# Optimization experiments

Hardware: AMD Instinct MI355X
Metric: run time of the kernel (lower is better)

## Reference

```python
import jax, jax.numpy as jnp
import numpy as np

D = 768       # model dim
H = 12        # num heads
DH = 64       # hidden_dim per head (D == H*DH)
DT = 32       # time_dim
KTEMP = 1.0   # k_temperature
LN_EPS = 1e-5


def setup_inputs() -> dict:
    key = jax.random.key(0)
    ks = jax.random.split(key, 10)
    B, T = 2, 2048
    states = jax.random.normal(ks[0], (B, T, D), jnp.float32)
    attention_mask = jnp.ones((B, T), jnp.int32)
    s = 0.02
    Wq = jax.random.normal(ks[1], (H * DH, D), jnp.float32) * s
    Wk = jax.random.normal(ks[2], (H * DH, D), jnp.float32) * s
    bk = jax.random.normal(ks[3], (H * DH,), jnp.float32) * s
    Wv = jax.random.normal(ks[4], (H * DH, D), jnp.float32) * s
    bv = jnp.zeros((H * DH,), jnp.float32)           # V.bias zeroed in __init__
    Wo = jax.random.normal(ks[5], (D, H * DH), jnp.float32) * s
    bo = jnp.zeros((D,), jnp.float32)                # O.bias zeroed in __init__
    q_bias = jnp.zeros((H * DH,), jnp.float32)
    time_angle = jax.random.uniform(ks[6], (H, DT), jnp.float32) ** 10 + 1e-8
    head_time_delta = jax.random.uniform(ks[7], (H,), jnp.float32)
    ln_gamma = jnp.ones((D,), jnp.float32)
    ln_beta = jnp.zeros((D,), jnp.float32)
    return {"states": states, "attention_mask": attention_mask,
            "Wq": Wq, "Wk": Wk, "bk": bk, "Wv": Wv, "bv": bv,
            "Wo": Wo, "bo": bo, "q_bias": q_bias,
            "time_angle": time_angle, "head_time_delta": head_time_delta,
            "ln_gamma": ln_gamma, "ln_beta": ln_beta}


def reference(states, attention_mask, Wq, Wk, bk, Wv, bv, Wo, bo, q_bias,
              time_angle, head_time_delta, ln_gamma, ln_beta):
    B, T, _ = states.shape
    dtype = states.dtype
    mask = attention_mask.astype(dtype)[..., None, None]  # B T 1 1

    inv_sqrt_dh = 1.0 / np.sqrt(DH).astype(np.float32)

    def get_time(delta):
        # delta: [1,H,1] or scalar 0.0
        pos = jnp.arange(T, dtype=dtype)[:, None, None]     # T 1 1
        ang = (pos + delta) * time_angle[None]              # T H Dt
        c, s = jnp.cos(ang), jnp.sin(ang)
        return jnp.concatenate([c + s, c - s], axis=-1) * inv_sqrt_dh  # T H 2Dt

    # --- q path ---
    q = states @ Wq.T - jnp.exp(q_bias)                     # B T (H*Dh), Q has no bias
    q = jax.nn.sigmoid(q.reshape(B, T, H, DH)) / DH * mask  # B T H Dh
    time_q = get_time(head_time_delta[None, :, None])       # T H 2Dt (with delta)
    time_k = get_time(0.0)                                  # T H 2Dt
    q_timed = q.sum(-1, keepdims=True) * time_q             # B T H 2Dt
    # scores: B T(query) L(key) H -- the large materialized tensor
    scores = jnp.einsum('bthd,lhd->btlh', q_timed, time_k)

    # --- kv path ---
    k = (states @ Wk.T + bk).reshape(B, T, H, DH) / KTEMP * mask
    v = (states @ Wv.T + bv).reshape(B, T, H, DH)
    kv = jax.nn.softmax(k, axis=-1) * v                     # B T H Dh

    # --- aggregate ---
    loading = jnp.einsum('btlh,blhd->bthd', scores, kv).reshape(B, T, D)
    attn_out = loading @ Wo.T + bo

    # residual + layernorm (dropout is identity in eval)
    x = states + attn_out
    mu = x.mean(-1, keepdims=True)
    var = x.var(-1, keepdims=True)
    return (x - mu) * jax.lax.rsqrt(var + LN_EPS) * ln_gamma + ln_beta
```

## Files before the change

kernel.cpp:

```cpp
#include <hip/hip_runtime.h>
#include <math.h>
#include <stdint.h>

#define TT 2048
#define BB 2
#define DD 768
#define HH 12
#define DHH 64
#define DTT 32
#define NROW 4096

typedef float v4 __attribute__((ext_vector_type(4)));
typedef __attribute__((ext_vector_type(8))) short s8v;
typedef __attribute__((ext_vector_type(4))) float f4v;
typedef unsigned short u16;
typedef __attribute__((ext_vector_type(4))) unsigned short us4;

__device__ __forceinline__ float wave_sum(float v) {
#pragma unroll
  for (int m = 32; m > 0; m >>= 1) v += __shfl_xor(v, m, 64);
  return v;
}
__device__ __forceinline__ float wave_max(float v) {
#pragma unroll
  for (int m = 32; m > 0; m >>= 1) v = fmaxf(v, __shfl_xor(v, m, 64));
  return v;
}
__device__ __forceinline__ u16 f2bf(float x) {
  unsigned u = __builtin_bit_cast(unsigned, x);
  u += 0x7fffu + ((u >> 16) & 1u);
  return (u16)(u >> 16);
}
__device__ __forceinline__ float bf2f(u16 b) {
  return __builtin_bit_cast(float, (unsigned)b << 16);
}
__device__ __forceinline__ void gload16(const void* g, void* l) {
  __builtin_amdgcn_global_load_lds(
      (const __attribute__((address_space(1))) unsigned int*)g,
      (__attribute__((address_space(3))) unsigned int*)l, 16, 0, 0);
}

__global__ __launch_bounds__(256) void time_tables(
    const float* __restrict__ tang, const float* __restrict__ hdelta,
    u16* __restrict__ timeqb, float* __restrict__ timek) {
  int idx = blockIdx.x * 256 + threadIdx.x;
  if (idx >= TT * HH * DTT) return;
  int d = idx % DTT;
  int h = (idx / DTT) % HH;
  int t = idx / (DTT * HH);
  float ang = tang[h * DTT + d];
  float sk, ck, sq, cq;
  sincosf((float)t * ang, &sk, &ck);
  sincosf(((float)t + hdelta[h]) * ang, &sq, &cq);
  timek[t * DD + h * DHH + d]       = (ck + sk) * 0.125f;
  timek[t * DD + h * DHH + d + DTT] = (ck - sk) * 0.125f;
  timeqb[t * DD + h * DHH + d]       = f2bf((cq + sq) * 0.125f);
  timeqb[t * DD + h * DHH + d + DTT] = f2bf((cq - sq) * 0.125f);
}

__global__ __launch_bounds__(256) void convert_bf16(
    const float* __restrict__ s, const float* __restrict__ wq,
    const float* __restrict__ wk, const float* __restrict__ wv,
    const float* __restrict__ wo, u16* __restrict__ sb,
    u16* __restrict__ wqkvb, u16* __restrict__ wob) {
  int idx = (blockIdx.x * 256 + threadIdx.x) * 4;
  const float* src;
  u16* dst;
  int off;
  if (idx < 3145728) { src = s; dst = sb; off = idx; }
  else if (idx < 3735552) { src = wq; dst = wqkvb; off = idx - 3145728; }
  else if (idx < 4325376) { src = wk; dst = wqkvb + 589824; off = idx - 3735552; }
  else if (idx < 4915200) { src = wv; dst = wqkvb + 1179648; off = idx - 4325376; }
  else { src = wo; dst = wob; off = idx - 4915200; }
  v4 f = *(const v4*)&src[off];
  us4 o;
#pragma unroll
  for (int j = 0; j < 4; ++j) o[j] = f2bf(f[j]);
  *(us4*)&dst[off] = o;
}

template <int EPI, int OBF>
__global__ __launch_bounds__(256) void gemm_bt(
    const u16* __restrict__ A, const u16* __restrict__ B, void* __restrict__ Cv,
    const float* __restrict__ bias, const float* __restrict__ res,
    int M, int N, int K) {
  __shared__ __align__(16) u16 As[2][4096];
  __shared__ __align__(16) u16 Bs[2][4096];
  const int tid = threadIdx.x;
  const int l = tid & 63;
  const int w = tid >> 6;
  const int wr = w >> 1, wc = w & 1;
  const int i0 = blockIdx.y * 128, j0 = blockIdx.x * 128;
  const int srow = tid >> 2, scol = (tid & 3) * 8;
  const u16* gA0 = A + (size_t)(i0 + srow) * K + scol;
  const u16* gA1 = gA0 + (size_t)64 * K;
  const u16* gB0 = B + (size_t)(j0 + srow) * K + scol;
  const u16* gB1 = gB0 + (size_t)64 * K;
  const int lo = tid * 8;

  f4v acc[4][4];
#pragma unroll
  for (int m = 0; m < 4; ++m)
#pragma unroll
    for (int n = 0; n < 4; ++n) acc[m][n] = (f4v){0.f, 0.f, 0.f, 0.f};

  gload16(gA0, &As[0][lo]);
  gload16(gA1, &As[0][2048 + lo]);
  gload16(gB0, &Bs[0][lo]);
  gload16(gB1, &Bs[0][2048 + lo]);

  const int KT = K >> 5;
  const int ar = wr * 64 + (l & 15);
  const int br = wc * 64 + (l & 15);
  const int kx = (l >> 4) * 8;
  int cur = 0;
  for (int kt = 0; kt < KT; ++kt) {
    __syncthreads();
    if (kt + 1 < KT) {
      int kb = (kt + 1) << 5;
      int nb = cur ^ 1;
      gload16(gA0 + kb, &As[nb][lo]);
      gload16(gA1 + kb, &As[nb][2048 + lo]);
      gload16(gB0 + kb, &Bs[nb][lo]);
      gload16(gB1 + kb, &Bs[nb][2048 + lo]);
    }
    s8v af[4], bf[4];
#pragma unroll
    for (int m = 0; m < 4; ++m)
      af[m] = *(const s8v*)&As[cur][(ar + m * 16) * 32 + kx];
#pragma unroll
    for (int n = 0; n < 4; ++n)
      bf[n] = *(const s8v*)&Bs[cur][(br + n * 16) * 32 + kx];
#pragma unroll
    for (int m = 0; m < 4; ++m)
#pragma unroll
      for (int n = 0; n < 4; ++n)
        acc[m][n] =
            __builtin_amdgcn_mfma_f32_16x16x32_bf16(af[m], bf[n], acc[m][n], 0, 0, 0);
    __syncthreads();
    cur ^= 1;
  }

  const int crow = i0 + wr * 64 + (l >> 4) * 4;
  const int ccol = j0 + wc * 64 + (l & 15);
#pragma unroll
  for (int m = 0; m < 4; ++m)
#pragma unroll
    for (int n = 0; n < 4; ++n) {
      int col = ccol + n * 16;
      size_t base = (size_t)(crow + m * 16) * N + col;
#pragma unroll
      for (int r = 0; r < 4; ++r) {
        float vv = acc[m][n][r];
        if (EPI) vv += bias[col] + res[base + (size_t)r * N];
        if (OBF)
          ((u16*)Cv)[base + (size_t)r * N] = f2bf(vv);
        else
          ((float*)Cv)[base + (size_t)r * N] = vv;
      }
    }
}

__global__ __launch_bounds__(256) void fuse_qkv(
    const u16* __restrict__ qkvb, const float* __restrict__ bk,
    const float* __restrict__ bv, const float* __restrict__ qb,
    const int* __restrict__ amask, float* __restrict__ kvout,
    float* __restrict__ qsum) {
  int w = (blockIdx.x << 2) + (threadIdx.x >> 6);
  int lane = threadIdx.x & 63;
  if (w >= NROW * HH) return;
  int h = w % HH;
  int i = w / HH;
  float mk = (float)amask[i];
  const u16* row = qkvb + (size_t)i * 2304;
  int col = h * DHH + lane;
  float qraw = bf2f(row[col]) - expf(qb[col]);
  float q = (1.f / (1.f + expf(-qraw))) * (1.0f / 64.0f) * mk;
  float qs = wave_sum(q);
  if (lane == 0) qsum[i * HH + h] = qs;
  float kval = (bf2f(row[768 + col]) + bk[col]) * mk;
  float kmax = wave_max(kval);
  float e = expf(kval - kmax);
  float es = wave_sum(e);
  float p = e / es;
  float vval = bf2f(row[1536 + col]) + bv[col];
  kvout[((size_t)i * HH + h) * DHH + lane] = p * vval;
}

__global__ __launch_bounds__(256) void calc_M(
    const float* __restrict__ timek, const float* __restrict__ kv,
    float* __restrict__ Mpart) {
  int blk = blockIdx.x;
  int split = blk & 15;
  int bh = blk >> 4;
  int b = bh / HH, h = bh % HH;
  __shared__ float Tk[64][68];
  __shared__ float Kv[64][68];
  int tid = threadIdx.x;
  int tx = tid & 15, ty = tid >> 4;
  float acc[4][4] = {};
  int t0 = split * 128;
  for (int tt = 0; tt < 128; tt += 64) {
#pragma unroll
    for (int p = 0; p < 4; ++p) {
      int f = tid + 256 * p;
      int r = f >> 4, c4 = (f & 15) << 2;
      int t = t0 + tt + r;
      *(v4*)&Tk[r][c4] = *(const v4*)&timek[(size_t)t * DD + h * DHH + c4];
      *(v4*)&Kv[r][c4] =
          *(const v4*)&kv[((size_t)(b * TT + t) * HH + h) * DHH + c4];
    }
    __syncthreads();
#pragma unroll
    for (int kk = 0; kk < 64; ++kk) {
      v4 a = *(const v4*)&Tk[kk][ty * 4];
      v4 bv4 = *(const v4*)&Kv[kk][tx * 4];
#pragma unroll
      for (int r = 0; r < 4; ++r)
#pragma unroll
        for (int c = 0; c < 4; ++c) acc[r][c] += a[r] * bv4[c];
    }
    __syncthreads();
  }
#pragma unroll
  for (int r = 0; r < 4; ++r)
#pragma unroll
    for (int c = 0; c < 4; ++c)
      Mpart[(size_t)blk * 4096 + (tx * 4 + c) * 64 + (ty * 4 + r)] = acc[r][c];
}

__global__ __launch_bounds__(256) void reduce_M(
    const float* __restrict__ Mpart, float* __restrict__ Mt) {
  int idx = blockIdx.x * 256 + threadIdx.x;
  int bh = idx >> 12;
  int p = idx & 4095;
  float s = 0.f;
#pragma unroll
  for (int sp = 0; sp < 16; ++sp)
    s += Mpart[(size_t)((bh << 4) + sp) * 4096 + p];
  Mt[(size_t)bh * 4096 + p] = s;
}

__global__ __launch_bounds__(256) void calc_loading_mfma(
    const u16* __restrict__ timeqb, const float* __restrict__ Mt,
    const float* __restrict__ qsum, u16* __restrict__ loading) {
  const int bh = blockIdx.y;
  const int b = bh / HH, h = bh % HH;
  const int t0 = blockIdx.x * 128;
  __shared__ __align__(16) u16 Ms[64 * 72];
  for (int p = threadIdx.x; p < 4096; p += 256)
    Ms[(p >> 6) * 72 + (p & 63)] = f2bf(Mt[(size_t)bh * 4096 + p]);
  __syncthreads();
  const int l = threadIdx.x & 63, w = threadIdx.x >> 6;
  f4v acc[2][4];
#pragma unroll
  for (int m = 0; m < 2; ++m)
#pragma unroll
    for (int n = 0; n < 4; ++n) acc[m][n] = (f4v){0.f, 0.f, 0.f, 0.f};
  const int arow = t0 + w * 32 + (l & 15);
  const int dcol = l & 15;
#pragma unroll
  for (int ks = 0; ks < 2; ++ks) {
    const int k0 = ks * 32 + (l >> 4) * 8;
    s8v af[2], bf[4];
#pragma unroll
    for (int m = 0; m < 2; ++m)
      af[m] = *(const s8v*)&timeqb[(size_t)(arow + m * 16) * DD + h * DHH + k0];
#pragma unroll
    for (int n = 0; n < 4; ++n)
      bf[n] = *(const s8v*)&Ms[(dcol + n * 16) * 72 + k0];
#pragma unroll
    for (int m = 0; m < 2; ++m)
#pragma unroll
      for (int n = 0; n < 4; ++n)
        acc[m][n] =
            __builtin_amdgcn_mfma_f32_16x16x32_bf16(af[m], bf[n], acc[m][n], 0, 0, 0);
  }
  const int trow = t0 + w * 32 + (l >> 4) * 4;
  float qs[2][4];
#pragma unroll
  for (int m = 0; m < 2; ++m)
#pragma unroll
    for (int r = 0; r < 4; ++r)
      qs[m][r] = qsum[(b * TT + trow + m * 16 + r) * HH + h];
#pragma unroll
  for (int m = 0; m < 2; ++m)
#pragma unroll
    for (int n = 0; n < 4; ++n)
#pragma unroll
      for (int r = 0; r < 4; ++r) {
        int i = b * TT + trow + m * 16 + r;
        loading[(size_t)i * DD + h * DHH + n * 16 + (l & 15)] =
            f2bf(qs[m][r] * acc[m][n][r]);
      }
}

__global__ __launch_bounds__(256) void layernorm(
    const float* __restrict__ X, const float* __restrict__ gamma,
    const float* __restrict__ beta, float* __restrict__ out) {
  int i = blockIdx.x;
  const float* x = X + (size_t)i * 768;
  float vals[3];
  float s = 0.f, s2 = 0.f;
#pragma unroll
  for (int p = 0; p < 3; ++p) {
    float v = x[threadIdx.x + 256 * p];
    vals[p] = v;
    s += v;
    s2 += v * v;
  }
  s = wave_sum(s);
  s2 = wave_sum(s2);
  __shared__ float red[8];
  int w = threadIdx.x >> 6;
  if ((threadIdx.x & 63) == 0) {
    red[w] = s;
    red[4 + w] = s2;
  }
  __syncthreads();
  float stot = red[0] + red[1] + red[2] + red[3];
  float s2tot = red[4] + red[5] + red[6] + red[7];
  float mu = stot * (1.f / 768.f);
  float var = s2tot * (1.f / 768.f) - mu * mu;
  float rs = rsqrtf(var + 1e-5f);
#pragma unroll
  for (int p = 0; p < 3; ++p) {
    int j = threadIdx.x + 256 * p;
    out[(size_t)i * 768 + j] = (vals[p] - mu) * rs * gamma[j] + beta[j];
  }
}

extern "C" void kernel_launch(void* const* d_in, const int* in_sizes, int n_in,
                              void* d_out, int out_size, void* d_ws,
                              size_t ws_size, hipStream_t stream) {
  const float* states = (const float*)d_in[0];
  const int* amask    = (const int*)d_in[1];
  const float* Wq     = (const float*)d_in[2];
  const float* Wk     = (const float*)d_in[3];
  const float* bk     = (const float*)d_in[4];
  const float* Wv     = (const float*)d_in[5];
  const float* bv     = (const float*)d_in[6];
  const float* Wo     = (const float*)d_in[7];
  const float* bo     = (const float*)d_in[8];
  const float* qb     = (const float*)d_in[9];
  const float* tang   = (const float*)d_in[10];
  const float* hdelta = (const float*)d_in[11];
  const float* gamma  = (const float*)d_in[12];
  const float* beta   = (const float*)d_in[13];
  float* out = (float*)d_out;
  float* ws = (float*)d_ws;

  u16* timeqb = (u16*)(ws);
  float* timek = ws + 786432;
  u16* qkvb   = (u16*)(ws + 2359296);
  u16* loadb  = (u16*)(ws + 2359296);
  float* xbuf = ws + 3932160;
  float* kvbuf = ws + 7077888;
  float* qsum = ws + 10223616;
  float* Mpart = ws + 10272768;
  float* Mt   = ws + 11845632;
  u16* Abf    = (u16*)(ws + 11943936);
  u16* Wqkvb  = (u16*)(ws + 13516800);
  u16* Wob    = (u16*)(ws + 14401536);

  time_tables<<<3072, 256, 0, stream>>>(tang, hdelta, timeqb, timek);
  convert_bf16<<<5376, 256, 0, stream>>>(states, Wq, Wk, Wv, Wo, Abf, Wqkvb, Wob);
  gemm_bt<0, 1><<<dim3(18, 32), 256, 0, stream>>>(Abf, Wqkvb, qkvb, nullptr,
                                                  nullptr, 4096, 2304, 768);
  fuse_qkv<<<12288, 256, 0, stream>>>(qkvb, bk, bv, qb, amask, kvbuf, qsum);
  calc_M<<<384, 256, 0, stream>>>(timek, kvbuf, Mpart);
  reduce_M<<<384, 256, 0, stream>>>(Mpart, Mt);
  calc_loading_mfma<<<dim3(16, 24), 256, 0, stream>>>(timeqb, Mt, qsum, loadb);
  gemm_bt<1, 0><<<dim3(6, 32), 256, 0, stream>>>(loadb, Wob, xbuf, bo, states,
                                                 4096, 768, 768);
  layernorm<<<4096, 256, 0, stream>>>(xbuf, gamma, beta, out);
}
```

Baseline: 103.8 us.

## Fuse q/kv epilogues into GEMMs, merge prep kernels, store intermediates as bf16

```diff
diff --git a/kernel.cpp b/kernel.cpp
--- a/kernel.cpp
+++ b/kernel.cpp
@@ -16,16 +16,6 @@
 typedef unsigned short u16;
 typedef __attribute__((ext_vector_type(4))) unsigned short us4;
 
-__device__ __forceinline__ float wave_sum(float v) {
-#pragma unroll
-  for (int m = 32; m > 0; m >>= 1) v += __shfl_xor(v, m, 64);
-  return v;
-}
-__device__ __forceinline__ float wave_max(float v) {
-#pragma unroll
-  for (int m = 32; m > 0; m >>= 1) v = fmaxf(v, __shfl_xor(v, m, 64));
-  return v;
-}
 __device__ __forceinline__ u16 f2bf(float x) {
   unsigned u = __builtin_bit_cast(unsigned, x);
   u += 0x7fffu + ((u >> 16) & 1u);
@@ -34,56 +24,73 @@
 __device__ __forceinline__ float bf2f(u16 b) {
   return __builtin_bit_cast(float, (unsigned)b << 16);
 }
+__device__ __forceinline__ float wave_sum(float v) {
+#pragma unroll
+  for (int m = 32; m > 0; m >>= 1) v += __shfl_xor(v, m, 64);
+  return v;
+}
 __device__ __forceinline__ void gload16(const void* g, void* l) {
   __builtin_amdgcn_global_load_lds(
       (const __attribute__((address_space(1))) unsigned int*)g,
       (__attribute__((address_space(3))) unsigned int*)l, 16, 0, 0);
 }
 
-__global__ __launch_bounds__(256) void time_tables(
+__global__ __launch_bounds__(256) void prep(
     const float* __restrict__ tang, const float* __restrict__ hdelta,
-    u16* __restrict__ timeqb, float* __restrict__ timek) {
-  int idx = blockIdx.x * 256 + threadIdx.x;
-  if (idx >= TT * HH * DTT) return;
-  int d = idx % DTT;
-  int h = (idx / DTT) % HH;
-  int t = idx / (DTT * HH);
-  float ang = tang[h * DTT + d];
-  float sk, ck, sq, cq;
-  sincosf((float)t * ang, &sk, &ck);
-  sincosf(((float)t + hdelta[h]) * ang, &sq, &cq);
-  timek[t * DD + h * DHH + d]       = (ck + sk) * 0.125f;
-  timek[t * DD + h * DHH + d + DTT] = (ck - sk) * 0.125f;
-  timeqb[t * DD + h * DHH + d]       = f2bf((cq + sq) * 0.125f);
-  timeqb[t * DD + h * DHH + d + DTT] = f2bf((cq - sq) * 0.125f);
-}
-
-__global__ __launch_bounds__(256) void convert_bf16(
     const float* __restrict__ s, const float* __restrict__ wq,
     const float* __restrict__ wk, const float* __restrict__ wv,
-    const float* __restrict__ wo, u16* __restrict__ sb,
-    u16* __restrict__ wqkvb, u16* __restrict__ wob) {
-  int idx = (blockIdx.x * 256 + threadIdx.x) * 4;
+    const float* __restrict__ wo, u16* __restrict__ timeqb,
+    u16* __restrict__ timekb, u16* __restrict__ sb, u16* __restrict__ wqb,
+    u16* __restrict__ wkvb, u16* __restrict__ wob) {
+  int bid = blockIdx.x;
+  if (bid < 3072) {
+    int idx = bid * 256 + threadIdx.x;
+    int d = idx % DTT;
+    int h = (idx / DTT) % HH;
+    int t = idx / (DTT * HH);
+    float ang = tang[h * DTT + d];
+    float sk, ck, sq, cq;
+    sincosf((float)t * ang, &sk, &ck);
+    sincosf(((float)t + hdelta[h]) * ang, &sq, &cq);
+    timekb[t * DD + h * DHH + d]       = f2bf((ck + sk) * 0.125f);
+    timekb[t * DD + h * DHH + d + DTT] = f2bf((ck - sk) * 0.125f);
+    timeqb[t * DD + h * DHH + d]       = f2bf((cq + sq) * 0.125f);
+    timeqb[t * DD + h * DHH + d + DTT] = f2bf((cq - sq) * 0.125f);
+    return;
+  }
+  int idx = (bid - 3072) * 256 + threadIdx.x;
+  int off = idx * 4;
   const float* src;
   u16* dst;
-  int off;
-  if (idx < 3145728) { src = s; dst = sb; off = idx; }
-  else if (idx < 3735552) { src = wq; dst = wqkvb; off = idx - 3145728; }
-  else if (idx < 4325376) { src = wk; dst = wqkvb + 589824; off = idx - 3735552; }
-  else if (idx < 4915200) { src = wv; dst = wqkvb + 1179648; off = idx - 4325376; }
-  else { src = wo; dst = wob; off = idx - 4915200; }
-  v4 f = *(const v4*)&src[off];
+  int so, dof;
+  if (off < 3145728) {
+    src = s; dst = sb; so = off; dof = off;
+  } else if (off < 3735552) {
+    src = wq; dst = wqb; so = off - 3145728; dof = so;
+  } else if (off < 4325376) {
+    src = wk; so = off - 3735552;
+    int j = so / 768, c = so - j * 768;
+    int h = j >> 6, r = j & 63;
+    dst = wkvb; dof = (h * 128 + r) * 768 + c;
+  } else if (off < 4915200) {
+    src = wv; so = off - 4325376;
+    int j = so / 768, c = so - j * 768;
+    int h = j >> 6, r = j & 63;
+    dst = wkvb; dof = (h * 128 + 64 + r) * 768 + c;
+  } else {
+    src = wo; dst = wob; so = off - 4915200; dof = so;
+  }
+  v4 f = *(const v4*)&src[so];
   us4 o;
 #pragma unroll
   for (int j = 0; j < 4; ++j) o[j] = f2bf(f[j]);
-  *(us4*)&dst[off] = o;
-}
-
-template <int EPI, int OBF>
-__global__ __launch_bounds__(256) void gemm_bt(
-    const u16* __restrict__ A, const u16* __restrict__ B, void* __restrict__ Cv,
-    const float* __restrict__ bias, const float* __restrict__ res,
-    int M, int N, int K) {
+  *(us4*)&dst[dof] = o;
+}
+
+__global__ __launch_bounds__(256) void gemm_q(
+    const u16* __restrict__ A, const u16* __restrict__ B,
+    const float* __restrict__ qb, const int* __restrict__ amask,
+    float* __restrict__ qsum) {
   __shared__ __align__(16) u16 As[2][4096];
   __shared__ __align__(16) u16 Bs[2][4096];
   const int tid = threadIdx.x;
@@ -92,31 +99,27 @@
   const int wr = w >> 1, wc = w & 1;
   const int i0 = blockIdx.y * 128, j0 = blockIdx.x * 128;
   const int srow = tid >> 2, scol = (tid & 3) * 8;
-  const u16* gA0 = A + (size_t)(i0 + srow) * K + scol;
-  const u16* gA1 = gA0 + (size_t)64 * K;
-  const u16* gB0 = B + (size_t)(j0 + srow) * K + scol;
-  const u16* gB1 = gB0 + (size_t)64 * K;
+  const u16* gA0 = A + (size_t)(i0 + srow) * 768 + scol;
+  const u16* gA1 = gA0 + (size_t)64 * 768;
+  const u16* gB0 = B + (size_t)(j0 + srow) * 768 + scol;
+  const u16* gB1 = gB0 + (size_t)64 * 768;
   const int lo = tid * 8;
-
   f4v acc[4][4];
 #pragma unroll
   for (int m = 0; m < 4; ++m)
 #pragma unroll
     for (int n = 0; n < 4; ++n) acc[m][n] = (f4v){0.f, 0.f, 0.f, 0.f};
-
   gload16(gA0, &As[0][lo]);
   gload16(gA1, &As[0][2048 + lo]);
   gload16(gB0, &Bs[0][lo]);
   gload16(gB1, &Bs[0][2048 + lo]);
-
-  const int KT = K >> 5;
   const int ar = wr * 64 + (l & 15);
   const int br = wc * 64 + (l & 15);
   const int kx = (l >> 4) * 8;
   int cur = 0;
-  for (int kt = 0; kt < KT; ++kt) {
-    __syncthreads();
-    if (kt + 1 < KT) {
+  for (int kt = 0; kt < 24; ++kt) {
+    __syncthreads();
+    if (kt + 1 < 24) {
       int kb = (kt + 1) << 5;
       int nb = cur ^ 1;
       gload16(gA0 + kb, &As[nb][lo]);
@@ -140,55 +143,133 @@
     __syncthreads();
     cur ^= 1;
   }
-
+  const int head = (j0 >> 6) + wc;
   const int crow = i0 + wr * 64 + (l >> 4) * 4;
-  const int ccol = j0 + wc * 64 + (l & 15);
+  float eqb[4];
+#pragma unroll
+  for (int n = 0; n < 4; ++n) eqb[n] = expf(qb[head * 64 + n * 16 + (l & 15)]);
 #pragma unroll
   for (int m = 0; m < 4; ++m)
 #pragma unroll
-    for (int n = 0; n < 4; ++n) {
-      int col = ccol + n * 16;
-      size_t base = (size_t)(crow + m * 16) * N + col;
+    for (int r = 0; r < 4; ++r) {
+      float ssum = 0.f;
+#pragma unroll
+      for (int n = 0; n < 4; ++n)
+        ssum += 1.f / (1.f + expf(-(acc[m][n][r] - eqb[n])));
+#pragma unroll
+      for (int mm = 8; mm > 0; mm >>= 1) ssum += __shfl_xor(ssum, mm, 64);
+      int row = crow + m * 16 + r;
+      if ((l & 15) == 0)
+        qsum[row * HH + head] = ssum * (float)amask[row] * (1.f / 64.f);
+    }
+}
+
+__global__ __launch_bounds__(256) void gemm_kv(
+    const u16* __restrict__ A, const u16* __restrict__ B,
+    const float* __restrict__ bk, const float* __restrict__ bv,
+    const int* __restrict__ amask, u16* __restrict__ kvb) {
+  __shared__ __align__(16) u16 As[2][4352];
+  __shared__ __align__(16) u16 Bs[2][4096];
+  const int tid = threadIdx.x;
+  const int l = tid & 63;
+  const int w = tid >> 6;
+  const int wr = w >> 1, wc = w & 1;
+  const int i0 = blockIdx.y * 128, j0 = blockIdx.x * 128;
+  const int head = blockIdx.x;
+  const int srow = tid >> 2, scol = (tid & 3) * 8;
+  const u16* gA0 = A + (size_t)(i0 + srow) * 768 + scol;
+  const u16* gA1 = gA0 + (size_t)64 * 768;
+  const u16* gB0 = B + (size_t)(j0 + srow) * 768 + scol;
+  const u16* gB1 = gB0 + (size_t)64 * 768;
+  const int lo = tid * 8;
+  f4v acc[4][4];
+#pragma unroll
+  for (int m = 0; m < 4; ++m)
+#pragma unroll
+    for (int n = 0; n < 4; ++n) acc[m][n] = (f4v){0.f, 0.f, 0.f, 0.f};
+  gload16(gA0, &As[0][lo]);
+  gload16(gA1, &As[0][2048 + lo]);
+  gload16(gB0, &Bs[0][lo]);
+  gload16(gB1, &Bs[0][2048 + lo]);
+  const int ar = wr * 64 + (l & 15);
+  const int br = wc * 64 + (l & 15);
+  const int kx = (l >> 4) * 8;
+  int cur = 0;
+  for (int kt = 0; kt < 24; ++kt) {
+    __syncthreads();
+    if (kt + 1 < 24) {
+      int kb = (kt + 1) << 5;
+      int nb = cur ^ 1;
+      gload16(gA0 + kb, &As[nb][lo]);
+      gload16(gA1 + kb, &As[nb][2048 + lo]);
+      gload16(gB0 + kb, &Bs[nb][lo]);
+      gload16(gB1 + kb, &Bs[nb][2048 + lo]);
+    }
+    s8v af[4], bf[4];
+#pragma unroll
+    for (int m = 0; m < 4; ++m)
+      af[m] = *(const s8v*)&As[cur][(ar + m * 16) * 32 + kx];
+#pragma unroll
+    for (int n = 0; n < 4; ++n)
+      bf[n] = *(const s8v*)&Bs[cur][(br + n * 16) * 32 + kx];
+#pragma unroll
+    for (int m = 0; m < 4; ++m)
+#pragma unroll
+      for (int n = 0; n < 4; ++n)
+        acc[m][n] =
+            __builtin_amdgcn_mfma_f32_16x16x32_bf16(af[m], bf[n], acc[m][n], 0, 0, 0);
+    __syncthreads();
+    cur ^= 1;
+  }
+  u16* Ps = &As[wr][0];
+  const int crow = i0 + wr * 64 + (l >> 4) * 4;
+  if (wc == 0) {
+#pragma unroll
+    for (int m = 0; m < 4; ++m)
 #pragma unroll
       for (int r = 0; r < 4; ++r) {
-        float vv = acc[m][n][r];
-        if (EPI) vv += bias[col] + res[base + (size_t)r * N];
-        if (OBF)
-          ((u16*)Cv)[base + (size_t)r * N] = f2bf(vv);
-        else
-          ((float*)Cv)[base + (size_t)r * N] = vv;
+        int row = crow + m * 16 + r;
+        float mk = (float)amask[row];
+        float kv4[4];
+#pragma unroll
+        for (int n = 0; n < 4; ++n)
+          kv4[n] = (acc[m][n][r] + bk[head * 64 + n * 16 + (l & 15)]) * mk;
+        float mx = fmaxf(fmaxf(kv4[0], kv4[1]), fmaxf(kv4[2], kv4[3]));
+#pragma unroll
+        for (int mm = 8; mm > 0; mm >>= 1) mx = fmaxf(mx, __shfl_xor(mx, mm, 64));
+        float e[4], es = 0.f;
+#pragma unroll
+        for (int n = 0; n < 4; ++n) { e[n] = expf(kv4[n] - mx); es += e[n]; }
+#pragma unroll
+        for (int mm = 8; mm > 0; mm >>= 1) es += __shfl_xor(es, mm, 64);
+        float inv = 1.f / es;
+        int lrow = (l >> 4) * 4 + m * 16 + r;
+#pragma unroll
+        for (int n = 0; n < 4; ++n)
+          Ps[lrow * 68 + n * 16 + (l & 15)] = f2bf(e[n] * inv);
       }
-    }
-}
-
-__global__ __launch_bounds__(256) void fuse_qkv(
-    const u16* __restrict__ qkvb, const float* __restrict__ bk,
-    const float* __restrict__ bv, const float* __restrict__ qb,
-    const int* __restrict__ amask, float* __restrict__ kvout,
-    float* __restrict__ qsum) {
-  int w = (blockIdx.x << 2) + (threadIdx.x >> 6);
-  int lane = threadIdx.x & 63;
-  if (w >= NROW * HH) return;
-  int h = w % HH;
-  int i = w / HH;
-  float mk = (float)amask[i];
-  const u16* row = qkvb + (size_t)i * 2304;
-  int col = h * DHH + lane;
-  float qraw = bf2f(row[col]) - expf(qb[col]);
-  float q = (1.f / (1.f + expf(-qraw))) * (1.0f / 64.0f) * mk;
-  float qs = wave_sum(q);
-  if (lane == 0) qsum[i * HH + h] = qs;
-  float kval = (bf2f(row[768 + col]) + bk[col]) * mk;
-  float kmax = wave_max(kval);
-  float e = expf(kval - kmax);
-  float es = wave_sum(e);
-  float p = e / es;
-  float vval = bf2f(row[1536 + col]) + bv[col];
-  kvout[((size_t)i * HH + h) * DHH + lane] = p * vval;
+  }
+  __syncthreads();
+  if (wc == 1) {
+#pragma unroll
+    for (int m = 0; m < 4; ++m)
+#pragma unroll
+      for (int r = 0; r < 4; ++r) {
+        int row = crow + m * 16 + r;
+        int lrow = (l >> 4) * 4 + m * 16 + r;
+#pragma unroll
+        for (int n = 0; n < 4; ++n) {
+          int d = n * 16 + (l & 15);
+          float p = bf2f(Ps[lrow * 68 + d]);
+          float vv = acc[m][n][r] + bv[head * 64 + d];
+          kvb[((size_t)row * HH + head) * 64 + d] = f2bf(p * vv);
+        }
+      }
+  }
 }
 
 __global__ __launch_bounds__(256) void calc_M(
-    const float* __restrict__ timek, const float* __restrict__ kv,
+    const u16* __restrict__ timekb, const u16* __restrict__ kvb,
     float* __restrict__ Mpart) {
   int blk = blockIdx.x;
   int split = blk & 15;
@@ -206,9 +287,13 @@
       int f = tid + 256 * p;
       int r = f >> 4, c4 = (f & 15) << 2;
       int t = t0 + tt + r;
-      *(v4*)&Tk[r][c4] = *(const v4*)&timek[(size_t)t * DD + h * DHH + c4];
-      *(v4*)&Kv[r][c4] =
-          *(const v4*)&kv[((size_t)(b * TT + t) * HH + h) * DHH + c4];
+      us4 tk = *(const us4*)&timekb[(size_t)t * DD + h * DHH + c4];
+      us4 kv = *(const us4*)&kvb[((size_t)(b * TT + t) * HH + h) * 64 + c4];
+#pragma unroll
+      for (int j = 0; j < 4; ++j) {
+        Tk[r][c4 + j] = bf2f(tk[j]);
+        Kv[r][c4 + j] = bf2f(kv[j]);
+      }
     }
     __syncthreads();
 #pragma unroll
@@ -230,7 +315,7 @@
 }
 
 __global__ __launch_bounds__(256) void reduce_M(
-    const float* __restrict__ Mpart, float* __restrict__ Mt) {
+    const float* __restrict__ Mpart, u16* __restrict__ Mtb) {
   int idx = blockIdx.x * 256 + threadIdx.x;
   int bh = idx >> 12;
   int p = idx & 4095;
@@ -238,18 +323,18 @@
 #pragma unroll
   for (int sp = 0; sp < 16; ++sp)
     s += Mpart[(size_t)((bh << 4) + sp) * 4096 + p];
-  Mt[(size_t)bh * 4096 + p] = s;
+  Mtb[(size_t)bh * 4096 + p] = f2bf(s);
 }
 
 __global__ __launch_bounds__(256) void calc_loading_mfma(
-    const u16* __restrict__ timeqb, const float* __restrict__ Mt,
+    const u16* __restrict__ timeqb, const u16* __restrict__ Mtb,
     const float* __restrict__ qsum, u16* __restrict__ loading) {
   const int bh = blockIdx.y;
   const int b = bh / HH, h = bh % HH;
   const int t0 = blockIdx.x * 128;
   __shared__ __align__(16) u16 Ms[64 * 72];
   for (int p = threadIdx.x; p < 4096; p += 256)
-    Ms[(p >> 6) * 72 + (p & 63)] = f2bf(Mt[(size_t)bh * 4096 + p]);
+    Ms[(p >> 6) * 72 + (p & 63)] = Mtb[(size_t)bh * 4096 + p];
   __syncthreads();
   const int l = threadIdx.x & 63, w = threadIdx.x >> 6;
   f4v acc[2][4];
@@ -293,6 +378,76 @@
         loading[(size_t)i * DD + h * DHH + n * 16 + (l & 15)] =
             f2bf(qs[m][r] * acc[m][n][r]);
       }
+}
+
+__global__ __launch_bounds__(256) void gemm_out(
+    const u16* __restrict__ A, const u16* __restrict__ B, float* __restrict__ C,
+    const float* __restrict__ bias, const float* __restrict__ res) {
+  __shared__ __align__(16) u16 As[2][4096];
+  __shared__ __align__(16) u16 Bs[2][4096];
+  const int tid = threadIdx.x;
+  const int l = tid & 63;
+  const int w = tid >> 6;
+  const int wr = w >> 1, wc = w & 1;
+  const int i0 = blockIdx.y * 128, j0 = blockIdx.x * 128;
+  const int srow = tid >> 2, scol = (tid & 3) * 8;
+  const u16* gA0 = A + (size_t)(i0 + srow) * 768 + scol;
+  const u16* gA1 = gA0 + (size_t)64 * 768;
+  const u16* gB0 = B + (size_t)(j0 + srow) * 768 + scol;
+  const u16* gB1 = gB0 + (size_t)64 * 768;
+  const int lo = tid * 8;
+  f4v acc[4][4];
+#pragma unroll
+  for (int m = 0; m < 4; ++m)
+#pragma unroll
+    for (int n = 0; n < 4; ++n) acc[m][n] = (f4v){0.f, 0.f, 0.f, 0.f};
+  gload16(gA0, &As[0][lo]);
+  gload16(gA1, &As[0][2048 + lo]);
+  gload16(gB0, &Bs[0][lo]);
+  gload16(gB1, &Bs[0][2048 + lo]);
+  const int ar = wr * 64 + (l & 15);
+  const int br = wc * 64 + (l & 15);
+  const int kx = (l >> 4) * 8;
+  int cur = 0;
+  for (int kt = 0; kt < 24; ++kt) {
+    __syncthreads();
+    if (kt + 1 < 24) {
+      int kb = (kt + 1) << 5;
+      int nb = cur ^ 1;
+      gload16(gA0 + kb, &As[nb][lo]);
+      gload16(gA1 + kb, &As[nb][2048 + lo]);
+      gload16(gB0 + kb, &Bs[nb][lo]);
+      gload16(gB1 + kb, &Bs[nb][2048 + lo]);
+    }
+    s8v af[4], bf[4];
+#pragma unroll
+    for (int m = 0; m < 4; ++m)
+      af[m] = *(const s8v*)&As[cur][(ar + m * 16) * 32 + kx];
+#pragma unroll
+    for (int n = 0; n < 4; ++n)
+      bf[n] = *(const s8v*)&Bs[cur][(br + n * 16) * 32 + kx];
+#pragma unroll
+    for (int m = 0; m < 4; ++m)
+#pragma unroll
+      for (int n = 0; n < 4; ++n)
+        acc[m][n] =
+            __builtin_amdgcn_mfma_f32_16x16x32_bf16(af[m], bf[n], acc[m][n], 0, 0, 0);
+    __syncthreads();
+    cur ^= 1;
+  }
+  const int crow = i0 + wr * 64 + (l >> 4) * 4;
+  const int ccol = j0 + wc * 64 + (l & 15);
+#pragma unroll
+  for (int m = 0; m < 4; ++m)
+#pragma unroll
+    for (int n = 0; n < 4; ++n) {
+      int col = ccol + n * 16;
+      size_t base = (size_t)(crow + m * 16) * 768 + col;
+#pragma unroll
+      for (int r = 0; r < 4; ++r)
+        C[base + (size_t)r * 768] =
+            acc[m][n][r] + bias[col] + res[base + (size_t)r * 768];
+    }
 }
 
 __global__ __launch_bounds__(256) void layernorm(
@@ -350,28 +505,26 @@
   float* out = (float*)d_out;
   float* ws = (float*)d_ws;
 
-  u16* timeqb = (u16*)(ws);
-  float* timek = ws + 786432;
-  u16* qkvb   = (u16*)(ws + 2359296);
-  u16* loadb  = (u16*)(ws + 2359296);
-  float* xbuf = ws + 3932160;
-  float* kvbuf = ws + 7077888;
-  float* qsum = ws + 10223616;
-  float* Mpart = ws + 10272768;
-  float* Mt   = ws + 11845632;
-  u16* Abf    = (u16*)(ws + 11943936);
-  u16* Wqkvb  = (u16*)(ws + 13516800);
-  u16* Wob    = (u16*)(ws + 14401536);
-
-  time_tables<<<3072, 256, 0, stream>>>(tang, hdelta, timeqb, timek);
-  convert_bf16<<<5376, 256, 0, stream>>>(states, Wq, Wk, Wv, Wo, Abf, Wqkvb, Wob);
-  gemm_bt<0, 1><<<dim3(18, 32), 256, 0, stream>>>(Abf, Wqkvb, qkvb, nullptr,
-                                                  nullptr, 4096, 2304, 768);
-  fuse_qkv<<<12288, 256, 0, stream>>>(qkvb, bk, bv, qb, amask, kvbuf, qsum);
-  calc_M<<<384, 256, 0, stream>>>(timek, kvbuf, Mpart);
-  reduce_M<<<384, 256, 0, stream>>>(Mpart, Mt);
-  calc_loading_mfma<<<dim3(16, 24), 256, 0, stream>>>(timeqb, Mt, qsum, loadb);
-  gemm_bt<1, 0><<<dim3(6, 32), 256, 0, stream>>>(loadb, Wob, xbuf, bo, states,
-                                                 4096, 768, 768);
+  u16* timeqb = (u16*)(ws + 0);
+  u16* timekb = (u16*)(ws + 786432);
+  u16* Abf    = (u16*)(ws + 1572864);
+  u16* Wqb    = (u16*)(ws + 3145728);
+  u16* Wkvb   = (u16*)(ws + 3440640);
+  u16* Wob    = (u16*)(ws + 4030464);
+  float* qsum = ws + 4325376;
+  u16* kvb    = (u16*)(ws + 4374528);
+  float* Mpart= ws + 5160960;
+  u16* Mtb    = (u16*)(ws + 6733824);
+  u16* loadb  = (u16*)(ws + 6758400);
+  float* xbuf = ws + 7544832;
+
+  prep<<<8448, 256, 0, stream>>>(tang, hdelta, states, Wq, Wk, Wv, Wo, timeqb,
+                                 timekb, Abf, Wqb, Wkvb, Wob);
+  gemm_q<<<dim3(6, 32), 256, 0, stream>>>(Abf, Wqb, qb, amask, qsum);
+  gemm_kv<<<dim3(12, 32), 256, 0, stream>>>(Abf, Wkvb, bk, bv, amask, kvb);
+  calc_M<<<384, 256, 0, stream>>>(timekb, kvb, Mpart);
+  reduce_M<<<384, 256, 0, stream>>>(Mpart, Mtb);
+  calc_loading_mfma<<<dim3(16, 24), 256, 0, stream>>>(timeqb, Mtb, qsum, loadb);
+  gemm_out<<<dim3(6, 32), 256, 0, stream>>>(loadb, Wob, xbuf, bo, states);
   layernorm<<<4096, 256, 0, stream>>>(xbuf, gamma, beta, out);
 }
```

Result: slower. 120.8 us (+16.4%).
